# Kernel tuning notes

Hardware: AMD Instinct MI355X
Metric: run time of the kernel (lower is better)

The kernel has to match this reference:

```python
import jax, jax.numpy as jnp
import numpy as np

B, S, W = 64, 128, 20
VOCAB, E, H = 256, 64, 256


def setup_inputs() -> dict:
    key = jax.random.key(0)
    ks = jax.random.split(key, 10)
    return {
        "chars": jax.random.randint(ks[0], (B, S, W), 0, VOCAB),
        "emb": jax.random.uniform(ks[1], (VOCAB, E), jnp.float32, -0.32, 0.32),
        "w1": jax.random.normal(ks[2], (H, E, 1), jnp.float32) * 0.1,
        "b1": jax.random.normal(ks[3], (H,), jnp.float32) * 0.1,
        "w3": jax.random.normal(ks[4], (H, E, 3), jnp.float32) * 0.1,
        "b3": jax.random.normal(ks[5], (H,), jnp.float32) * 0.1,
        "w5": jax.random.normal(ks[6], (H, E, 5), jnp.float32) * 0.1,
        "b5": jax.random.normal(ks[7], (H,), jnp.float32) * 0.1,
        "lw": jax.random.normal(ks[8], (H, 3 * H), jnp.float32) * 0.05,
        "lb": jax.random.normal(ks[9], (H,), jnp.float32) * 0.05,
    }


def _conv_relu_maxpool(x, w, b):
    # x: [N, E, W], w: [H, E, k] ('same' padding k//2) -> [N, H]
    k = w.shape[-1]
    pad = k // 2
    y = jax.lax.conv_general_dilated(
        x, w, window_strides=(1,), padding=[(pad, pad)],
        dimension_numbers=("NCH", "OIH", "NCH"))
    y = jax.nn.relu(y + b[None, :, None])
    return jnp.max(y, axis=2)  # global max over char positions


def reference(chars, emb, w1, b1, w3, b3, w5, b5, lw, lb):
    b, s, wlen = chars.shape
    flat = chars.reshape(-1, wlen)                 # [N, W]
    x = emb[flat]                                  # [N, W, E]
    x = jnp.transpose(x, (0, 2, 1))                # [N, E, W]
    outs = jnp.concatenate([
        _conv_relu_maxpool(x, w1, b1),
        _conv_relu_maxpool(x, w3, b3),
        _conv_relu_maxpool(x, w5, b5),
    ], axis=1)                                     # [N, 3H]
    out = outs @ lw.T + lb                         # [N, H]
    return out.reshape(b, s, -1)
```

## Files before the change

kernel.cpp:

```cpp
#include <hip/hip_runtime.h>
#include <hip/hip_bf16.h>

#define BB 64
#define SS 128
#define WW 20
#define NW (BB*SS)
#define VOCAB 256
#define EE 64
#define HH 256
#define K3 (3*HH)
#define NTAP 9
#define UNIT 2304

typedef short bf16x8 __attribute__((ext_vector_type(8)));
typedef float f32x4  __attribute__((ext_vector_type(4)));

__device__ __forceinline__ ushort f2bs(float x) {
    __hip_bfloat16 h = __float2bfloat16(x);
    union { __hip_bfloat16 h; ushort u; } c; c.h = h; return c.u;
}
__device__ __forceinline__ float blo(unsigned u) {
    union { unsigned i; float f; } c; c.i = u << 16; return c.f;
}
__device__ __forceinline__ float bhi(unsigned u) {
    union { unsigned i; float f; } c; c.i = u & 0xffff0000u; return c.f;
}

#define SET4(d, w0, w1) { d[0]=blo(w0); d[1]=bhi(w0); d[2]=blo(w1); d[3]=bhi(w1); }
#define ADD4(d, w0, w1) { d[0]+=blo(w0); d[1]+=bhi(w0); d[2]+=blo(w1); d[3]+=bhi(w1); }
#define MAX4(m, s) { m[0]=fmaxf(m[0],s[0]); m[1]=fmaxf(m[1],s[1]); \
                     m[2]=fmaxf(m[2],s[2]); m[3]=fmaxf(m[3],s[3]); }


__global__ __launch_bounds__(256) void transpose_w(
        const float* __restrict__ w1,
        const float* __restrict__ w3,
        const float* __restrict__ w5,
        float* __restrict__ wT) {
    int idx = blockIdx.x * 256 + threadIdx.x;
    int tap = idx >> 14;
    int e   = (idx >> 8) & 63;
    int h   = idx & 255;
    float v;
    if (tap == 0)      v = w1[h*EE + e];
    else if (tap <= 3) v = w3[(h*EE + e)*3 + (tap-1)];
    else               v = w5[(h*EE + e)*5 + (tap-4)];
    wT[idx] = v;
}

__global__ __launch_bounds__(256) void build_tables(
        const float* __restrict__ emb,
        const float* __restrict__ wT,
        ushort* __restrict__ P2) {
    __shared__ float emb_s[2][EE];
    const int v0  = blockIdx.x * 2;
    const int tap = blockIdx.y;
    const int h   = threadIdx.x;
    if (h < 2*EE) emb_s[h >> 6][h & 63] = emb[v0*EE + h];
    __syncthreads();

    float a0 = 0.f, a1 = 0.f;
    const float* wp = wT + (tap*EE)*HH + h;
    #pragma unroll 8
    for (int e = 0; e < EE; ++e) {
        float w = wp[e*HH];
        a0 += emb_s[0][e] * w;
        a1 += emb_s[1][e] * w;
    }
    const int g = h >> 2, r = h & 3;
    const int base = (tap < 8) ? ((tap>>1)*512 + g*8 + (tap&1)*4 + r)
                               : (2048 + g*4 + r);
    P2[(v0+0)*UNIT + base] = f2bs(a0);
    P2[(v0+1)*UNIT + base] = f2bs(a1);
}

__global__ __launch_bounds__(256) void conv_pool(
        const int* __restrict__ chars,
        const ushort* __restrict__ P2,
        const float* __restrict__ b1,
        const float* __restrict__ b3,
        const float* __restrict__ b5,
        ushort* __restrict__ outs) {
    const int tid  = threadIdx.x;
    const int wave = tid >> 6, lane = tid & 63;
    const int n    = blockIdx.x * 4 + wave;
    const char* Pb = (const char*)P2;

    const int* cp = chars + n * WW;
    int c[WW];
    #pragma unroll
    for (int j = 0; j < WW; ++j) c[j] = cp[j];

    float acc3[3][4], acc5[5][4], m1[4], m3[4], m5[4];
    #pragma unroll
    for (int i = 0; i < 4; ++i) {
        acc3[0][i] = 0.f; acc5[0][i] = 0.f; acc5[1][i] = 0.f;
        m1[i] = -1e30f; m3[i] = -1e30f; m5[i] = -1e30f;
    }

    uint4 q[2][4]; uint2 e8[2];
    {
        const char* p = Pb + (size_t)c[0] * 4608;
        #pragma unroll
        for (int i = 0; i < 4; ++i) q[0][i] = *(const uint4*)(p + i*1024 + lane*16);
        e8[0] = *(const uint2*)(p + 4096 + lane*8);
    }

    #pragma unroll
    for (int j = 0; j < WW; ++j) {
        const int cur = j & 1, nxt = cur ^ 1;
        if (j + 1 < WW) {
            const char* p = Pb + (size_t)c[j+1] * 4608;
            #pragma unroll
            for (int i = 0; i < 4; ++i) q[nxt][i] = *(const uint4*)(p + i*1024 + lane*16);
            e8[nxt] = *(const uint2*)(p + 4096 + lane*8);
        }
        uint4 q0 = q[cur][0], q1 = q[cur][1], q2 = q[cur][2], q3 = q[cur][3];
        uint2 ee = e8[cur];

        m1[0] = fmaxf(m1[0], blo(q0.x)); m1[1] = fmaxf(m1[1], bhi(q0.x));
        m1[2] = fmaxf(m1[2], blo(q0.y)); m1[3] = fmaxf(m1[3], bhi(q0.y));
        if (j + 1 < WW) SET4(acc3[(j+1)%3], q0.z, q0.w)
        ADD4(acc3[j%3], q1.x, q1.y)
        if (j >= 1) { ADD4(acc3[(j-1)%3], q1.z, q1.w)
                      MAX4(m3, acc3[(j-1)%3]) }
        if (j + 2 < WW) SET4(acc5[(j+2)%5], q2.x, q2.y)
        if (j + 1 < WW) ADD4(acc5[(j+1)%5], q2.z, q2.w)
        ADD4(acc5[j%5], q3.x, q3.y)
        if (j >= 1) ADD4(acc5[(j-1)%5], q3.z, q3.w)
        if (j >= 2) { ADD4(acc5[(j-2)%5], ee.x, ee.y)
                      MAX4(m5, acc5[(j-2)%5]) }
    }
    MAX4(m3, acc3[(WW-1)%3])
    MAX4(m5, acc5[(WW-2)%5])
    MAX4(m5, acc5[(WW-1)%5])

    const int h4 = lane * 4;
    float4 bb1 = *(const float4*)(b1 + h4);
    float4 bb3 = *(const float4*)(b3 + h4);
    float4 bb5 = *(const float4*)(b5 + h4);
    ushort* op = outs + (size_t)n * K3 + h4;
    ushort4 o;
    o.x = f2bs(fmaxf(m1[0]+bb1.x, 0.f)); o.y = f2bs(fmaxf(m1[1]+bb1.y, 0.f));
    o.z = f2bs(fmaxf(m1[2]+bb1.z, 0.f)); o.w = f2bs(fmaxf(m1[3]+bb1.w, 0.f));
    *(ushort4*)(op + 0*HH) = o;
    o.x = f2bs(fmaxf(m3[0]+bb3.x, 0.f)); o.y = f2bs(fmaxf(m3[1]+bb3.y, 0.f));
    o.z = f2bs(fmaxf(m3[2]+bb3.z, 0.f)); o.w = f2bs(fmaxf(m3[3]+bb3.w, 0.f));
    *(ushort4*)(op + 1*HH) = o;
    o.x = f2bs(fmaxf(m5[0]+bb5.x, 0.f)); o.y = f2bs(fmaxf(m5[1]+bb5.y, 0.f));
    o.z = f2bs(fmaxf(m5[2]+bb5.z, 0.f)); o.w = f2bs(fmaxf(m5[3]+bb5.w, 0.f));
    *(ushort4*)(op + 2*HH) = o;
}

__global__ __launch_bounds__(256) void cvt_lw(
        const float* __restrict__ lw, ushort* __restrict__ lwb) {
    int i = (blockIdx.x * 256 + threadIdx.x) * 4;
    float4 v = *(const float4*)(lw + i);
    ushort4 o;
    o.x = f2bs(v.x); o.y = f2bs(v.y); o.z = f2bs(v.z); o.w = f2bs(v.w);
    *(ushort4*)(lwb + i) = o;
}

__global__ __launch_bounds__(64) void gemm_out(
        const ushort* __restrict__ outs,
        const ushort* __restrict__ lwb,
        const float* __restrict__ lb,
        float* __restrict__ out) {
    const int lane = threadIdx.x;
    const int m0 = blockIdx.x * 16;
    const int n0 = blockIdx.y * 32;
    const int mrow = lane & 15, quad = lane >> 4;

    f32x4 acc0 = (f32x4){0.f,0.f,0.f,0.f}, acc1 = (f32x4){0.f,0.f,0.f,0.f};
    const ushort* arow = outs + (size_t)(m0 + mrow) * K3 + quad * 8;
    const ushort* brow = lwb  + (size_t)(n0 + mrow) * K3 + quad * 8;

    bf16x8 a_c  = *(const bf16x8*)arow;
    bf16x8 b_c0 = *(const bf16x8*)brow;
    bf16x8 b_c1 = *(const bf16x8*)(brow + 16*K3);

    #pragma unroll
    for (int it = 0; it < K3/32; ++it) {
        const int kn = (it + 1 < K3/32) ? (it + 1) * 32 : 0;
        bf16x8 a_n  = *(const bf16x8*)(arow + kn);
        bf16x8 b_n0 = *(const bf16x8*)(brow + kn);
        bf16x8 b_n1 = *(const bf16x8*)(brow + 16*K3 + kn);
        acc0 = __builtin_amdgcn_mfma_f32_16x16x32_bf16(a_c, b_c0, acc0, 0, 0, 0);
        acc1 = __builtin_amdgcn_mfma_f32_16x16x32_bf16(a_c, b_c1, acc1, 0, 0, 0);
        a_c = a_n; b_c0 = b_n0; b_c1 = b_n1;
    }

    #pragma unroll
    for (int nn = 0; nn < 2; ++nn) {
        const f32x4 acc = nn ? acc1 : acc0;
        int ncol = n0 + nn*16 + mrow;
        float lbv = lb[ncol];
        #pragma unroll
        for (int r = 0; r < 4; ++r)
            out[(size_t)(m0 + quad*4 + r)*HH + ncol] = acc[r] + lbv;
    }
}

extern "C" void kernel_launch(void* const* d_in, const int* in_sizes, int n_in,
                              void* d_out, int out_size, void* d_ws, size_t ws_size,
                              hipStream_t stream) {
    const int*   chars = (const int*)d_in[0];
    const float* emb   = (const float*)d_in[1];
    const float* w1    = (const float*)d_in[2];
    const float* b1    = (const float*)d_in[3];
    const float* w3    = (const float*)d_in[4];
    const float* b3    = (const float*)d_in[5];
    const float* w5    = (const float*)d_in[6];
    const float* b5    = (const float*)d_in[7];
    const float* lw    = (const float*)d_in[8];
    const float* lb    = (const float*)d_in[9];

    ushort* P2   = (ushort*)d_ws;
    float*  wT   = (float*)(P2 + VOCAB * UNIT);
    ushort* outs = (ushort*)(wT + NTAP * EE * HH);
    ushort* lwb  = outs + (size_t)NW * K3;

    transpose_w<<<(NTAP*EE*HH)/256, 256, 0, stream>>>(w1, w3, w5, wT);
    cvt_lw<<<(HH*K3)/1024, 256, 0, stream>>>(lw, lwb);
    build_tables<<<dim3(VOCAB/2, NTAP), 256, 0, stream>>>(emb, wT, P2);
    conv_pool<<<NW/4, 256, 0, stream>>>(chars, P2, b1, b3, b5, outs);
    gemm_out<<<dim3(NW/16, HH/32), 64, 0, stream>>>(outs, lwb, lb, (float*)d_out);
}
```

Baseline: 150.4 us.

## Fuse prep kernels, coalesce table writes, scalarize char loads, widen GEMM tile

```diff
diff --git a/kernel.cpp b/kernel.cpp
--- a/kernel.cpp
+++ b/kernel.cpp
@@ -32,46 +32,59 @@
                      m[2]=fmaxf(m[2],s[2]); m[3]=fmaxf(m[3],s[3]); }
 
 
-__global__ __launch_bounds__(256) void transpose_w(
+__global__ __launch_bounds__(256) void prep(
         const float* __restrict__ w1,
         const float* __restrict__ w3,
         const float* __restrict__ w5,
-        float* __restrict__ wT) {
-    int idx = blockIdx.x * 256 + threadIdx.x;
-    int tap = idx >> 14;
-    int e   = (idx >> 8) & 63;
-    int h   = idx & 255;
-    float v;
-    if (tap == 0)      v = w1[h*EE + e];
-    else if (tap <= 3) v = w3[(h*EE + e)*3 + (tap-1)];
-    else               v = w5[(h*EE + e)*5 + (tap-4)];
-    wT[idx] = v;
+        const float* __restrict__ lw,
+        float* __restrict__ wTp,
+        ushort* __restrict__ lwb) {
+    const int bid = blockIdx.x;
+    if (bid < 576) {
+        int idx = bid * 256 + threadIdx.x;
+        int e = idx / UNIT;
+        int j = idx - e * UNIT;
+        int tap, h;
+        if (j < 2048) {
+            int chunk = j >> 9, w = j & 511, p = w & 7;
+            tap = chunk * 2 + (p >> 2);
+            h   = (w >> 3) * 4 + (p & 3);
+        } else { tap = 8; h = j - 2048; }
+        float v;
+        if (tap == 0)      v = w1[h*EE + e];
+        else if (tap <= 3) v = w3[(h*EE + e)*3 + (tap-1)];
+        else               v = w5[(h*EE + e)*5 + (tap-4)];
+        wTp[idx] = v;
+    } else {
+        int i = ((bid - 576) * 256 + threadIdx.x) * 4;
+        float4 v = *(const float4*)(lw + i);
+        ushort4 o;
+        o.x = f2bs(v.x); o.y = f2bs(v.y); o.z = f2bs(v.z); o.w = f2bs(v.w);
+        *(ushort4*)(lwb + i) = o;
+    }
 }
 
 __global__ __launch_bounds__(256) void build_tables(
         const float* __restrict__ emb,
-        const float* __restrict__ wT,
+        const float* __restrict__ wTp,
         ushort* __restrict__ P2) {
     __shared__ float emb_s[2][EE];
-    const int v0  = blockIdx.x * 2;
-    const int tap = blockIdx.y;
-    const int h   = threadIdx.x;
-    if (h < 2*EE) emb_s[h >> 6][h & 63] = emb[v0*EE + h];
+    const int v0 = blockIdx.x * 2;
+    const int j  = blockIdx.y * 256 + threadIdx.x;
+    const int t  = threadIdx.x;
+    if (t < 2*EE) emb_s[t >> 6][t & 63] = emb[v0*EE + t];
     __syncthreads();
 
     float a0 = 0.f, a1 = 0.f;
-    const float* wp = wT + (tap*EE)*HH + h;
+    const float* wp = wTp + j;
     #pragma unroll 8
     for (int e = 0; e < EE; ++e) {
-        float w = wp[e*HH];
+        float w = wp[e * UNIT];
         a0 += emb_s[0][e] * w;
         a1 += emb_s[1][e] * w;
     }
-    const int g = h >> 2, r = h & 3;
-    const int base = (tap < 8) ? ((tap>>1)*512 + g*8 + (tap&1)*4 + r)
-                               : (2048 + g*4 + r);
-    P2[(v0+0)*UNIT + base] = f2bs(a0);
-    P2[(v0+1)*UNIT + base] = f2bs(a1);
+    P2[(size_t)(v0+0)*UNIT + j] = f2bs(a0);
+    P2[(size_t)(v0+1)*UNIT + j] = f2bs(a1);
 }
 
 __global__ __launch_bounds__(256) void conv_pool(
@@ -89,7 +102,7 @@
     const int* cp = chars + n * WW;
     int c[WW];
     #pragma unroll
-    for (int j = 0; j < WW; ++j) c[j] = cp[j];
+    for (int j = 0; j < WW; ++j) c[j] = __builtin_amdgcn_readfirstlane(cp[j]);
 
     float acc3[3][4], acc5[5][4], m1[4], m3[4], m5[4];
     #pragma unroll
@@ -152,52 +165,50 @@
     *(ushort4*)(op + 2*HH) = o;
 }
 
-__global__ __launch_bounds__(256) void cvt_lw(
-        const float* __restrict__ lw, ushort* __restrict__ lwb) {
-    int i = (blockIdx.x * 256 + threadIdx.x) * 4;
-    float4 v = *(const float4*)(lw + i);
-    ushort4 o;
-    o.x = f2bs(v.x); o.y = f2bs(v.y); o.z = f2bs(v.z); o.w = f2bs(v.w);
-    *(ushort4*)(lwb + i) = o;
-}
-
 __global__ __launch_bounds__(64) void gemm_out(
         const ushort* __restrict__ outs,
         const ushort* __restrict__ lwb,
         const float* __restrict__ lb,
         float* __restrict__ out) {
     const int lane = threadIdx.x;
-    const int m0 = blockIdx.x * 16;
+    const int m0 = blockIdx.x * 32;
     const int n0 = blockIdx.y * 32;
     const int mrow = lane & 15, quad = lane >> 4;
 
-    f32x4 acc0 = (f32x4){0.f,0.f,0.f,0.f}, acc1 = (f32x4){0.f,0.f,0.f,0.f};
-    const ushort* arow = outs + (size_t)(m0 + mrow) * K3 + quad * 8;
-    const ushort* brow = lwb  + (size_t)(n0 + mrow) * K3 + quad * 8;
-
-    bf16x8 a_c  = *(const bf16x8*)arow;
-    bf16x8 b_c0 = *(const bf16x8*)brow;
-    bf16x8 b_c1 = *(const bf16x8*)(brow + 16*K3);
+    f32x4 acc00 = (f32x4){0,0,0,0}, acc01 = (f32x4){0,0,0,0};
+    f32x4 acc10 = (f32x4){0,0,0,0}, acc11 = (f32x4){0,0,0,0};
+    const ushort* ap = outs + (size_t)(m0 + mrow) * K3 + quad * 8;
+    const ushort* bp = lwb  + (size_t)(n0 + mrow) * K3 + quad * 8;
+
+    bf16x8 a0 = *(const bf16x8*)ap, a1 = *(const bf16x8*)(ap + 16*K3);
+    bf16x8 b0 = *(const bf16x8*)bp, b1 = *(const bf16x8*)(bp + 16*K3);
 
     #pragma unroll
     for (int it = 0; it < K3/32; ++it) {
         const int kn = (it + 1 < K3/32) ? (it + 1) * 32 : 0;
-        bf16x8 a_n  = *(const bf16x8*)(arow + kn);
-        bf16x8 b_n0 = *(const bf16x8*)(brow + kn);
-        bf16x8 b_n1 = *(const bf16x8*)(brow + 16*K3 + kn);
-        acc0 = __builtin_amdgcn_mfma_f32_16x16x32_bf16(a_c, b_c0, acc0, 0, 0, 0);
-        acc1 = __builtin_amdgcn_mfma_f32_16x16x32_bf16(a_c, b_c1, acc1, 0, 0, 0);
-        a_c = a_n; b_c0 = b_n0; b_c1 = b_n1;
-    }
-
-    #pragma unroll
-    for (int nn = 0; nn < 2; ++nn) {
-        const f32x4 acc = nn ? acc1 : acc0;
-        int ncol = n0 + nn*16 + mrow;
-        float lbv = lb[ncol];
+        bf16x8 a0n = *(const bf16x8*)(ap + kn);
+        bf16x8 a1n = *(const bf16x8*)(ap + 16*K3 + kn);
+        bf16x8 b0n = *(const bf16x8*)(bp + kn);
+        bf16x8 b1n = *(const bf16x8*)(bp + 16*K3 + kn);
+        acc00 = __builtin_amdgcn_mfma_f32_16x16x32_bf16(a0, b0, acc00, 0, 0, 0);
+        acc01 = __builtin_amdgcn_mfma_f32_16x16x32_bf16(a0, b1, acc01, 0, 0, 0);
+        acc10 = __builtin_amdgcn_mfma_f32_16x16x32_bf16(a1, b0, acc10, 0, 0, 0);
+        acc11 = __builtin_amdgcn_mfma_f32_16x16x32_bf16(a1, b1, acc11, 0, 0, 0);
+        a0 = a0n; a1 = a1n; b0 = b0n; b1 = b1n;
+    }
+
+    #pragma unroll
+    for (int i = 0; i < 2; ++i) {
         #pragma unroll
-        for (int r = 0; r < 4; ++r)
-            out[(size_t)(m0 + quad*4 + r)*HH + ncol] = acc[r] + lbv;
+        for (int jn = 0; jn < 2; ++jn) {
+            const f32x4 acc = (i==0) ? (jn==0 ? acc00 : acc01)
+                                     : (jn==0 ? acc10 : acc11);
+            int ncol = n0 + jn*16 + mrow;
+            float lbv = lb[ncol];
+            #pragma unroll
+            for (int r = 0; r < 4; ++r)
+                out[(size_t)(m0 + i*16 + quad*4 + r)*HH + ncol] = acc[r] + lbv;
+        }
     }
 }
 
@@ -216,13 +227,12 @@
     const float* lb    = (const float*)d_in[9];
 
     ushort* P2   = (ushort*)d_ws;
-    float*  wT   = (float*)(P2 + VOCAB * UNIT);
-    ushort* outs = (ushort*)(wT + NTAP * EE * HH);
+    float*  wTp  = (float*)(P2 + VOCAB * UNIT);
+    ushort* outs = (ushort*)(wTp + EE * UNIT);
     ushort* lwb  = outs + (size_t)NW * K3;
 
-    transpose_w<<<(NTAP*EE*HH)/256, 256, 0, stream>>>(w1, w3, w5, wT);
-    cvt_lw<<<(HH*K3)/1024, 256, 0, stream>>>(lw, lwb);
-    build_tables<<<dim3(VOCAB/2, NTAP), 256, 0, stream>>>(emb, wT, P2);
+    prep<<<768, 256, 0, stream>>>(w1, w3, w5, lw, wTp, lwb);
+    build_tables<<<dim3(VOCAB/2, NTAP), 256, 0, stream>>>(emb, wTp, P2);
     conv_pool<<<NW/4, 256, 0, stream>>>(chars, P2, b1, b3, b5, outs);
-    gemm_out<<<dim3(NW/16, HH/32), 64, 0, stream>>>(outs, lwb, lb, (float*)d_out);
-}
+    gemm_out<<<dim3(NW/32, HH/32), 64, 0, stream>>>(outs, lwb, lb, (float*)d_out);
+}
```

Measured after the change: 141.5 us. 5.9% less time.
